# Optimization experiments

Measured on AMD Instinct MI355X. Metric: run time of the kernel, lower is better.

## Reference

```python
import jax, jax.numpy as jnp
import numpy as np

DIM = 64          # hidden dim
EDGE_DIM = 6      # edge feature dim
A = 6             # action_dim (torsion bins); also torsions per graph
B = 512           # num_graphs
NPG = 40          # nodes per graph
N = B * NPG       # 20480 nodes
E = 43008         # edges
T = B * A         # 3072 total torsions


def _lin_init(k, out_f, in_f):
    bound = 1.0 / np.sqrt(in_f)
    kw, kb = jax.random.split(k)
    w = jax.random.uniform(kw, (out_f, in_f), jnp.float32, -bound, bound)
    b = jax.random.uniform(kb, (out_f,), jnp.float32, -bound, bound)
    return w, b


def setup_inputs() -> dict:
    key = jax.random.key(0)
    ks = jax.random.split(key, 24)
    inp = {}
    inp['x'] = jax.random.normal(ks[0], (N, 3), jnp.float32)
    inp['edge_attr'] = jax.random.uniform(ks[1], (E, EDGE_DIM), jnp.float32)
    inp['edge_index'] = jax.random.randint(ks[2], (2, E), 0, N)
    inp['batch'] = jnp.arange(N, dtype=jnp.int32) // NPG            # graph-sorted
    inp['nrbidx'] = jnp.repeat(jnp.arange(B, dtype=jnp.int32), A)   # torsion -> graph
    inp['nonring'] = jax.random.randint(ks[3], (T, 4), 0, N)        # 4 atoms per torsion
    # parameters
    inp['lin0_w'], inp['lin0_b'] = _lin_init(ks[4], DIM, 3)
    inp['enn1_w'], inp['enn1_b'] = _lin_init(ks[5], DIM, EDGE_DIM)
    inp['enn2_w'], inp['enn2_b'] = _lin_init(ks[6], DIM * DIM, DIM)
    inp['root_w'] = jax.random.uniform(ks[7], (DIM, DIM), jnp.float32, -1/np.sqrt(DIM), 1/np.sqrt(DIM))
    inp['conv_b'] = jnp.zeros((DIM,), jnp.float32)
    inp['gru_w_ih'], inp['gru_b_ih'] = _lin_init(ks[8], 3 * DIM, DIM)
    inp['gru_w_hh'], inp['gru_b_hh'] = _lin_init(ks[9], 3 * DIM, DIM)
    inp['s2s_w_ih'], inp['s2s_b_ih'] = _lin_init(ks[10], 4 * DIM, 2 * DIM)
    inp['s2s_w_hh'], inp['s2s_b_hh'] = _lin_init(ks[11], 4 * DIM, DIM)
    inp['mem_w_ih'], inp['mem_b_ih'] = _lin_init(ks[12], 4 * DIM, 2 * DIM)
    inp['mem_w_hh'], inp['mem_b_hh'] = _lin_init(ks[13], 4 * DIM, DIM)
    inp['lin1_w'], inp['lin1_b'] = _lin_init(ks[14], DIM, 5 * DIM)
    inp['lin2_w'], inp['lin2_b'] = _lin_init(ks[15], A, DIM)
    return inp


def _lstm_cell(xin, hc, w_ih, w_hh, b_ih, b_hh):
    h, c = hc
    g = xin @ w_ih.T + b_ih + h @ w_hh.T + b_hh
    i, f, gg, o = jnp.split(g, 4, axis=-1)
    c2 = jax.nn.sigmoid(f) * c + jax.nn.sigmoid(i) * jnp.tanh(gg)
    h2 = jax.nn.sigmoid(o) * jnp.tanh(c2)
    return h2, (h2, c2)


def reference(x, edge_attr, lin0_w, lin0_b, enn1_w, enn1_b, enn2_w, enn2_b,
              root_w, conv_b, gru_w_ih, gru_b_ih, gru_w_hh, gru_b_hh,
              s2s_w_ih, s2s_b_ih, s2s_w_hh, s2s_b_hh,
              mem_w_ih, mem_b_ih, mem_w_hh, mem_b_hh,
              lin1_w, lin1_b, lin2_w, lin2_b,
              edge_index, batch, nrbidx, nonring):
    dim = DIM
    out = jax.nn.relu(x @ lin0_w.T + lin0_b)                         # (N, dim)
    # edge-conditioned weights (constant across the 6 iterations)
    ew = jax.nn.relu(edge_attr @ enn1_w.T + enn1_b)
    W = (ew @ enn2_w.T + enn2_b).reshape(-1, dim, dim)               # (E, dim, dim)
    src, dst = edge_index[0], edge_index[1]
    deg = jax.ops.segment_sum(jnp.ones_like(src, jnp.float32), dst, num_segments=N)
    denom = jnp.maximum(deg, 1.0)[:, None]
    h = out                                                          # GRU hidden
    for _ in range(6):
        msg = jnp.einsum('ei,eio->eo', out[src], W)                  # gather + bmm
        agg = jax.ops.segment_sum(msg, dst, num_segments=N) / denom  # scatter-mean
        m = jax.nn.relu(agg + out @ root_w + conv_b)                 # NNConv out
        gi = m @ gru_w_ih.T + gru_b_ih
        gh = h @ gru_w_hh.T + gru_b_hh
        ir, iz, inn = jnp.split(gi, 3, axis=-1)
        hr, hz, hn = jnp.split(gh, 3, axis=-1)
        r = jax.nn.sigmoid(ir + hr)
        z = jax.nn.sigmoid(iz + hz)
        n = jnp.tanh(inn + r * hn)
        h = (1.0 - z) * n + z * h
        out = h
    # Set2Set pooling (processing_steps=6)
    q_star = jnp.zeros((B, 2 * dim), out.dtype)
    hc = (jnp.zeros((B, dim), out.dtype), jnp.zeros((B, dim), out.dtype))
    for _ in range(6):
        q, hc = _lstm_cell(q_star, hc, s2s_w_ih, s2s_w_hh, s2s_b_ih, s2s_b_hh)
        e = jnp.sum(out * q[batch], axis=-1)                         # (N,)
        emax = jax.ops.segment_max(e, batch, num_segments=B)
        a = jnp.exp(e - emax[batch])
        a = a / jax.ops.segment_sum(a, batch, num_segments=B)[batch]
        r = jax.ops.segment_sum(a[:, None] * out, batch, num_segments=B)
        q_star = jnp.concatenate([q, r], axis=-1)                    # (B, 2*dim)
    # memory LSTM, one step, zero initial state
    hc0 = (jnp.zeros((B, dim), out.dtype), jnp.zeros((B, dim), out.dtype))
    lstm_out, (hx, cx) = _lstm_cell(q_star, hc0, mem_w_ih, mem_w_hh, mem_b_ih, mem_b_hh)
    t = lstm_out[nrbidx].reshape(B, 1, A, dim)
    nd = out[nonring.reshape(-1)].reshape(B, 4, A, dim)
    z2 = jnp.concatenate([t, nd], axis=1)                            # (B, 5, A, dim)
    z2 = jnp.transpose(z2, (0, 3, 2, 1)).reshape(-1, 5 * dim)        # (T, 5*dim)
    z2 = jax.nn.relu(z2 @ lin1_w.T + lin1_b)
    z2 = z2 @ lin2_w.T + lin2_b                                      # (T, A)
    logit = z2.reshape(B, A, A)   # equal torsion counts -> pad_sequence == reshape
    return (logit, hx[None], cx[None])
```

## Files before the change

kernel.cpp:

```cpp
#include <hip/hip_runtime.h>
#include <hip/hip_fp16.h>

#define NN 20480
#define EE 43008
#define BB 512
#define TT 3072

typedef _Float16 f16;
typedef _Float16 f16x8 __attribute__((ext_vector_type(8)));
typedef float f32x4 __attribute__((ext_vector_type(4)));

__device__ __forceinline__ float sigm(float x) { return 1.0f / (1.0f + __expf(-x)); }
__device__ __forceinline__ float tanh_f(float x) {
    float xc = fminf(fmaxf(x, -15.f), 15.f);
    float t = __expf(2.f * xc);
    return (t - 1.f) / (t + 1.f);
}

__global__ void k_prep0(const float* __restrict__ x, const float* __restrict__ ea,
                        const float* __restrict__ l0w, const float* __restrict__ l0b,
                        const float* __restrict__ e1w, const float* __restrict__ e1b,
                        const float* __restrict__ e2w, const float* __restrict__ e2b,
                        const float* __restrict__ gwih, const float* __restrict__ gwhh,
                        const float* __restrict__ swih, const float* __restrict__ swhh,
                        const float* __restrict__ mwih,
                        float* __restrict__ feat, f16* __restrict__ feat16, f16* __restrict__ ew16,
                        f16* __restrict__ qmtp, float* __restrict__ deg,
                        float* __restrict__ wihT, float* __restrict__ whhT,
                        float* __restrict__ s2sihT, float* __restrict__ s2shhT,
                        float* __restrict__ memihT)
{
    const int S0 = NN;
    const int S1 = S0 + NN * 64;
    const int S2 = S1 + EE * 64;
    const int S3 = S2 + 130 * 256 * 8;
    const int S4 = S3 + 64 * 192;
    const int S5 = S4 + 64 * 192;
    const int S6 = S5 + 128 * 256;
    const int S7 = S6 + 64 * 256;
    const int S8 = S7 + 128 * 256;
    for (int idx = blockIdx.x * blockDim.x + threadIdx.x; idx < S8; idx += gridDim.x * blockDim.x) {
        if (idx < S0) {
            deg[idx] = 0.f;
        } else if (idx < S1) {
            int t = idx - S0; int n = t >> 6, o = t & 63;
            float v = l0b[o] + x[n * 3] * l0w[o * 3] + x[n * 3 + 1] * l0w[o * 3 + 1] + x[n * 3 + 2] * l0w[o * 3 + 2];
            v = fmaxf(v, 0.f);
            feat[t] = v; feat16[t] = (f16)v;
        } else if (idx < S2) {
            int t = idx - S1; int e = t >> 6, o = t & 63;
            float acc = e1b[o];
#pragma unroll
            for (int j = 0; j < 6; ++j) acc += ea[e * 6 + j] * e1w[o * 6 + j];
            ew16[t] = (f16)fmaxf(acc, 0.f);
        } else if (idx < S3) {
            int t = idx - S2;
            int j = t & 7;
            int lane = (t >> 3) & 63;
            int cc = t >> 9;
            int c = cc >> 2, ct = cc & 3;
            int n = (ct << 4) | (lane & 15);
            int col = c * 32 + ((lane >> 4) << 3) + j;
            float v;
            if (col < 4096) v = e2w[(((col >> 6) << 6) + n) * 64 + (col & 63)];
            else            v = e2b[(col - 4096) * 64 + n];
            qmtp[t] = (f16)v;
        } else if (idx < S4) { int t = idx - S3; int i = t / 192, g = t - i * 192; wihT[t] = gwih[g * 64 + i]; }
        else if (idx < S5)   { int t = idx - S4; int i = t / 192, g = t - i * 192; whhT[t] = gwhh[g * 64 + i]; }
        else if (idx < S6)   { int t = idx - S5; int k = t >> 8, j = t & 255; s2sihT[t] = swih[j * 128 + k]; }
        else if (idx < S7)   { int t = idx - S6; int k = t >> 8, j = t & 255; s2shhT[t] = swhh[j * 64 + k]; }
        else                 { int t = idx - S7; int k = t >> 8, j = t & 255; memihT[t] = mwih[j * 128 + k]; }
    }
}

__global__ void k_prep1(const int* __restrict__ dstp, float* __restrict__ deg)
{
    int e = blockIdx.x * blockDim.x + threadIdx.x;
    if (e < EE) atomicAdd(&deg[dstp[e]], 1.0f);
}

__global__ __launch_bounds__(1024) void k_scan(const float* __restrict__ deg,
                                               int* __restrict__ rowptr, int* __restrict__ fill)
{
    __shared__ int part[1024];
    const int t = threadIdx.x;
    const int base = t * 20;
    int local[20];
    int s = 0;
#pragma unroll
    for (int j = 0; j < 20; ++j) { local[j] = s; s += (int)deg[base + j]; }
    part[t] = s;
    __syncthreads();
    for (int off = 1; off < 1024; off <<= 1) {
        int u = (t >= off) ? part[t - off] : 0;
        __syncthreads();
        part[t] += u;
        __syncthreads();
    }
    const int coff = part[t] - s;
#pragma unroll
    for (int j = 0; j < 20; ++j) { rowptr[base + j] = coff + local[j]; fill[base + j] = 0; }
    if (t == 1023) rowptr[NN] = part[1023];
}

__global__ void k_fill(const int* __restrict__ dstp, const int* __restrict__ rowptr,
                       int* __restrict__ fill, int* __restrict__ eidx)
{
    int e = blockIdx.x * blockDim.x + threadIdx.x;
    if (e < EE) {
        int d = dstp[e];
        int slot = atomicAdd(&fill[d], 1);
        eidx[rowptr[d] + slot] = e;
    }
}

__global__ __launch_bounds__(256, 3) void k_msg(const f16* __restrict__ feat16, const f16* __restrict__ ew16,
                                                const f16* __restrict__ qmtp,
                                                const int* __restrict__ srcp,
                                                float* __restrict__ msg)
{
    __shared__ f16 s_lds[64 * 64];
    __shared__ f16 w_lds[64 * 64];
    __shared__ float cmb[2][64][36];
    const int tid = threadIdx.x;
    const int e0 = blockIdx.x * 64;
    {
        int row = tid >> 2, q = tid & 3;
        int sn = srcp[e0 + row];
        const uint4* gs = (const uint4*)(feat16 + (size_t)sn * 64 + q * 16);
        const uint4* gw = (const uint4*)(ew16 + (size_t)(e0 + row) * 64 + q * 16);
        uint4 s0v = gs[0], s1v = gs[1];
        uint4 w0v = gw[0], w1v = gw[1];
        char* sbw = (char*)s_lds;
        char* wbw = (char*)w_lds;
        int swz = (row & 7) << 4;
        *(uint4*)(sbw + row * 128 + ((q * 32) ^ swz)) = s0v;
        *(uint4*)(sbw + row * 128 + ((q * 32 + 16) ^ swz)) = s1v;
        *(uint4*)(wbw + row * 128 + ((q * 32) ^ swz)) = w0v;
        *(uint4*)(wbw + row * 128 + ((q * 32 + 16) ^ swz)) = w1v;
    }
    __syncthreads();
    const int wv = tid >> 6, l = tid & 63;
    const int lh = l >> 4, ll = l & 15;
    const int cp = wv & 1;
    const int kp = wv >> 1;
    const int ctb = cp * 2;
    const char* sb = (const char*)s_lds;
    const char* wb = (const char*)w_lds;
    int rowv[4], swzv[4];
#pragma unroll
    for (int rg = 0; rg < 4; ++rg) { rowv[rg] = rg * 16 + ll; swzv[rg] = (rowv[rg] & 7) << 4; }
    f16x8 wf[4][2];
#pragma unroll
    for (int rg = 0; rg < 4; ++rg) {
        wf[rg][0] = *(const f16x8*)(wb + rowv[rg] * 128 + ((lh * 16) ^ swzv[rg]));
        wf[rg][1] = *(const f16x8*)(wb + rowv[rg] * 128 + ((64 + lh * 16) ^ swzv[rg]));
    }
    const f16x8* base = (const f16x8*)qmtp + l;
    f32x4 acc[4][2] = {};
    const int i0 = kp * 32;
    f16x8 S[3][2][2];
#pragma unroll
    for (int pp = 0; pp < 3; ++pp)
#pragma unroll
        for (int ab = 0; ab < 2; ++ab)
#pragma unroll
            for (int j = 0; j < 2; ++j)
                S[pp][ab][j] = base[((2 * (i0 + pp) + ab) * 4 + ctb + j) * 64];
    f16x8 sc[4];
#pragma unroll
    for (int p = 0; p < 32; ++p) {
        if ((p & 7) == 0) {
#pragma unroll
            for (int rg = 0; rg < 4; ++rg)
                sc[rg] = *(const f16x8*)(sb + rowv[rg] * 128 + ((((i0 + p) * 2)) ^ swzv[rg]));
        }
        const int bi = p % 3;
        __builtin_amdgcn_s_setprio(1);
#pragma unroll
        for (int rg = 0; rg < 4; ++rg) {
            f16 s = sc[rg][p & 7];
            f16x8 a0, a1;
#pragma unroll
            for (int j8 = 0; j8 < 8; ++j8) { a0[j8] = wf[rg][0][j8] * s; a1[j8] = wf[rg][1][j8] * s; }
#pragma unroll
            for (int j = 0; j < 2; ++j) {
                acc[rg][j] = __builtin_amdgcn_mfma_f32_16x16x32_f16(a0, S[bi][0][j], acc[rg][j], 0, 0, 0);
                acc[rg][j] = __builtin_amdgcn_mfma_f32_16x16x32_f16(a1, S[bi][1][j], acc[rg][j], 0, 0, 0);
            }
        }
        __builtin_amdgcn_s_setprio(0);
        int inext = i0 + p + 3; if (inext > 64) inext = 64;
#pragma unroll
        for (int ab = 0; ab < 2; ++ab)
#pragma unroll
            for (int j = 0; j < 2; ++j)
                S[bi][ab][j] = base[((2 * inext + ab) * 4 + ctb + j) * 64];
    }
    if (kp == 1) {
#pragma unroll
        for (int rg = 0; rg < 4; ++rg) {
            f16x8 sf0 = *(const f16x8*)(sb + rowv[rg] * 128 + ((lh * 16) ^ swzv[rg]));
            f16x8 sf1 = *(const f16x8*)(sb + rowv[rg] * 128 + ((64 + lh * 16) ^ swzv[rg]));
#pragma unroll
            for (int j = 0; j < 2; ++j) {
                acc[rg][j] = __builtin_amdgcn_mfma_f32_16x16x32_f16(sf0, S[2][0][j], acc[rg][j], 0, 0, 0);
                acc[rg][j] = __builtin_amdgcn_mfma_f32_16x16x32_f16(sf1, S[2][1][j], acc[rg][j], 0, 0, 0);
            }
        }
#pragma unroll
        for (int rg = 0; rg < 4; ++rg)
#pragma unroll
            for (int j = 0; j < 2; ++j)
#pragma unroll
                for (int q = 0; q < 4; ++q)
                    cmb[cp][rg * 16 + lh * 4 + q][j * 16 + ll] = acc[rg][j][q];
    }
    __syncthreads();
    if (kp == 0) {
#pragma unroll
        for (int rg = 0; rg < 4; ++rg)
#pragma unroll
            for (int q = 0; q < 4; ++q) {
                int r = rg * 16 + lh * 4 + q;
#pragma unroll
                for (int j = 0; j < 2; ++j) {
                    float v = acc[rg][j][q] + cmb[cp][r][j * 16 + ll];
                    msg[(size_t)(e0 + r) * 64 + ctb * 16 + j * 16 + ll] = v;
                }
            }
    }
}

__global__ __launch_bounds__(256) void k_node(float* __restrict__ feat, f16* __restrict__ feat16,
                                              const float* __restrict__ msg, const int* __restrict__ rowptr,
                                              const int* __restrict__ eidx, const float* __restrict__ deg,
                                              const float* __restrict__ root_w, const float* __restrict__ conv_b,
                                              const float* __restrict__ wihT, const float* __restrict__ whhT,
                                              const float* __restrict__ bih, const float* __restrict__ bhh)
{
    __shared__ float h_lds[4][4][64];
    __shared__ float m_lds[4][4][64];
    const int wv = threadIdx.x >> 6, l = threadIdx.x & 63;
    const int nb = blockIdx.x * 16 + wv * 4;
    float h[4], m[4];
#pragma unroll
    for (int nd = 0; nd < 4; ++nd) {
        int n = nb + nd;
        float hv = feat[(size_t)n * 64 + l];
        h[nd] = hv; h_lds[wv][nd][l] = hv;
        int r0 = rowptr[n], r1 = rowptr[n + 1];
        float a = 0.f;
        for (int r = r0; r < r1; ++r) {
            int e = eidx[r];
            a += msg[(size_t)e * 64 + l];
        }
        float inv = 1.0f / fmaxf(deg[n], 1.0f);
        m[nd] = a * inv + conv_b[l];
    }
    __syncthreads();
    for (int i = 0; i < 64; ++i) {
        float w = root_w[i * 64 + l];
#pragma unroll
        for (int nd = 0; nd < 4; ++nd) m[nd] += h_lds[wv][nd][i] * w;
    }
#pragma unroll
    for (int nd = 0; nd < 4; ++nd) { m[nd] = fmaxf(m[nd], 0.f); m_lds[wv][nd][l] = m[nd]; }
    __syncthreads();
    float g0[4], g1[4], g2[4], G0[4], G1[4], G2[4];
#pragma unroll
    for (int nd = 0; nd < 4; ++nd) {
        g0[nd] = bih[l]; g1[nd] = bih[64 + l]; g2[nd] = bih[128 + l];
        G0[nd] = bhh[l]; G1[nd] = bhh[64 + l]; G2[nd] = bhh[128 + l];
    }
    for (int i = 0; i < 64; ++i) {
        float wi0 = wihT[i * 192 + l], wi1 = wihT[i * 192 + 64 + l], wi2 = wihT[i * 192 + 128 + l];
        float wh0 = whhT[i * 192 + l], wh1 = whhT[i * 192 + 64 + l], wh2 = whhT[i * 192 + 128 + l];
#pragma unroll
        for (int nd = 0; nd < 4; ++nd) {
            float mb = m_lds[wv][nd][i], hb = h_lds[wv][nd][i];
            g0[nd] += mb * wi0; g1[nd] += mb * wi1; g2[nd] += mb * wi2;
            G0[nd] += hb * wh0; G1[nd] += hb * wh1; G2[nd] += hb * wh2;
        }
    }
#pragma unroll
    for (int nd = 0; nd < 4; ++nd) {
        int n = nb + nd;
        float r = sigm(g0[nd] + G0[nd]);
        float z = sigm(g1[nd] + G1[nd]);
        float nn2 = tanh_f(g2[nd] + r * G2[nd]);
        float hn = (1.f - z) * nn2 + z * h[nd];
        feat[(size_t)n * 64 + l] = hn;
        feat16[(size_t)n * 64 + l] = (f16)hn;
    }
}

__global__ __launch_bounds__(512) void k_s2s(const float* __restrict__ feat,
                                             const float* __restrict__ s2sihT, const float* __restrict__ s2shhT,
                                             const float* __restrict__ sbih, const float* __restrict__ sbhh,
                                             const float* __restrict__ memihT,
                                             const float* __restrict__ mbih, const float* __restrict__ mbhh,
                                             float* __restrict__ lstm_out, float* __restrict__ dout)
{
    __shared__ float ft[2][64][49];
    __shared__ float qs[2][128];
    __shared__ float hh[2][64];
    __shared__ float cc[2][64];
    __shared__ float qv[2][64];
    __shared__ float g0p[2][256];
    __shared__ float g1p[2][256];
    const int t = threadIdx.x;
    const int g0 = blockIdx.x * 2;
    for (int i = t; i < 2 * 40 * 64; i += 512) {
        int g = i / 2560;
        int rem = i - g * 2560;
        int row = rem >> 6, o = rem & 63;
        ft[g][o][row] = feat[((size_t)(g0 + g) * 40 + row) * 64 + o];
    }
    if (t < 256) qs[t >> 7][t & 127] = 0.f;
    if (t < 128) { hh[t >> 6][t & 63] = 0.f; cc[t >> 6][t & 63] = 0.f; }
    __syncthreads();
    const int jj = t & 255;
    const int half = t >> 8;
    const int gg = t >> 6, gl = t & 63;
    const float b_s = sbih[jj] + sbhh[jj];
    const float b_m = mbih[jj] + mbhh[jj];
    for (int step = 0; step < 7; ++step) {
        const bool mem = (step == 6);
        {
            float a0, a1;
            if (!mem) {
                if (half == 0) {
                    a0 = b_s; a1 = b_s;
#pragma unroll 16
                    for (int k = 0; k < 96; ++k) {
                        float w = s2sihT[k * 256 + jj];
                        a0 += qs[0][k] * w;
                        a1 += qs[1][k] * w;
                    }
                } else {
                    a0 = 0.f; a1 = 0.f;
#pragma unroll 16
                    for (int k = 96; k < 128; ++k) {
                        float w = s2sihT[k * 256 + jj];
                        a0 += qs[0][k] * w;
                        a1 += qs[1][k] * w;
                    }
#pragma unroll 16
                    for (int k = 0; k < 64; ++k) {
                        float w = s2shhT[k * 256 + jj];
                        a0 += hh[0][k] * w;
                        a1 += hh[1][k] * w;
                    }
                }
            } else {
                if (half == 0) {
                    a0 = b_m; a1 = b_m;
#pragma unroll 16
                    for (int k = 0; k < 64; ++k) {
                        float w = memihT[k * 256 + jj];
                        a0 += qs[0][k] * w;
                        a1 += qs[1][k] * w;
                    }
                } else {
                    a0 = 0.f; a1 = 0.f;
#pragma unroll 16
                    for (int k = 64; k < 128; ++k) {
                        float w = memihT[k * 256 + jj];
                        a0 += qs[0][k] * w;
                        a1 += qs[1][k] * w;
                    }
                }
            }
            if (half == 0) { g0p[0][jj] = a0; g0p[1][jj] = a1; }
            else           { g1p[0][jj] = a0; g1p[1][jj] = a1; }
        }
        __syncthreads();
        if (t < 128) {
            float ii = sigm(g0p[gg][gl]        + g1p[gg][gl]);
            float ff = sigm(g0p[gg][64 + gl]   + g1p[gg][64 + gl]);
            float g2 = tanh_f(g0p[gg][128 + gl] + g1p[gg][128 + gl]);
            float oo = sigm(g0p[gg][192 + gl]  + g1p[gg][192 + gl]);
            float cprev = mem ? 0.f : cc[gg][gl];
            float c2 = ff * cprev + ii * g2;
            float h2 = oo * tanh_f(c2);
            if (!mem) {
                cc[gg][gl] = c2; hh[gg][gl] = h2;
                qv[gg][gl] = h2; qs[gg][gl] = h2;
                const int g = gg, l = gl;
                float e = -1e30f;
                if (l < 40) {
                    float s = 0.f;
                    for (int o = 0; o < 64; ++o) s += ft[g][o][l] * qv[g][o];
                    e = s;
                }
                float emax = e;
#pragma unroll
                for (int off = 32; off; off >>= 1) emax = fmaxf(emax, __shfl_xor(emax, off));
                float av = (l < 40) ? __expf(e - emax) : 0.f;
                float asum = av;
#pragma unroll
                for (int off = 32; off; off >>= 1) asum += __shfl_xor(asum, off);
                av /= asum;
                float r = 0.f;
                for (int nd = 0; nd < 40; ++nd) r += __shfl(av, nd) * ft[g][l][nd];
                qs[g][64 + l] = r;
            } else {
                int gidx = g0 + gg;
                lstm_out[(size_t)gidx * 64 + gl] = h2;
                dout[18432 + (size_t)gidx * 64 + gl] = h2;
                dout[18432 + 32768 + (size_t)gidx * 64 + gl] = c2;
            }
        }
        __syncthreads();
    }
}

__global__ __launch_bounds__(256) void k_final(const float* __restrict__ feat,
                                               const float* __restrict__ lstm_out,
                                               const int* __restrict__ nrbidx, const int* __restrict__ nonring,
                                               const float* __restrict__ l1w, const float* __restrict__ l1b,
                                               const float* __restrict__ l2w, const float* __restrict__ l2b,
                                               float* __restrict__ dout)
{
    __shared__ float z_lds[4][320];
    __shared__ float y_lds[4][64];
    const int wv = threadIdx.x >> 6, l = threadIdx.x & 63;
    const int r = blockIdx.x * 4 + wv;
    const int b = r / 6, rr = r - b * 6;
#pragma unroll
    for (int p = 0; p < 5; ++p) {
        int c = p * 64 + l;
        int f2 = rr * 320 + c;
        int d = f2 / 30;
        int rem = f2 - d * 30;
        int a = rem / 5;
        int s = rem - a * 5;
        float v;
        if (s == 0) v = lstm_out[(size_t)nrbidx[b * 6 + a] * 64 + d];
        else {
            int atom = nonring[b * 24 + (s - 1) * 6 + a];
            v = feat[(size_t)atom * 64 + d];
        }
        z_lds[wv][c] = v;
    }
    __syncthreads();
    {
        float acc = l1b[l];
        const float4* wr = (const float4*)(l1w + (size_t)l * 320);
        const float4* zr = (const float4*)(z_lds[wv]);
        for (int c4 = 0; c4 < 80; ++c4) {
            float4 w4 = wr[c4]; float4 z4 = zr[c4];
            acc += w4.x * z4.x + w4.y * z4.y + w4.z * z4.z + w4.w * z4.w;
        }
        y_lds[wv][l] = fmaxf(acc, 0.f);
    }
    __syncthreads();
    if (l < 6) {
        float acc = l2b[l];
        const float* yr = y_lds[wv];
        const float* w2 = l2w + l * 64;
        for (int o = 0; o < 64; ++o) acc += yr[o] * w2[o];
        dout[b * 36 + rr * 6 + l] = acc;
    }
}

extern "C" void kernel_launch(void* const* d_in, const int* in_sizes, int n_in,
                              void* d_out, int out_size, void* d_ws, size_t ws_size,
                              hipStream_t stream)
{
    const float* x    = (const float*)d_in[0];
    const float* ea   = (const float*)d_in[1];
    const int*   ei   = (const int*)d_in[2];
    const int*   nrb  = (const int*)d_in[4];
    const int*   nonr = (const int*)d_in[5];
    const float* l0w  = (const float*)d_in[6];  const float* l0b = (const float*)d_in[7];
    const float* e1w  = (const float*)d_in[8];  const float* e1b = (const float*)d_in[9];
    const float* e2w  = (const float*)d_in[10]; const float* e2b = (const float*)d_in[11];
    const float* rootw= (const float*)d_in[12]; const float* convb = (const float*)d_in[13];
    const float* gwih = (const float*)d_in[14]; const float* gbih = (const float*)d_in[15];
    const float* gwhh = (const float*)d_in[16]; const float* gbhh = (const float*)d_in[17];
    const float* swih = (const float*)d_in[18]; const float* sbih = (const float*)d_in[19];
    const float* swhh = (const float*)d_in[20]; const float* sbhh = (const float*)d_in[21];
    const float* mwih = (const float*)d_in[22]; const float* mbih = (const float*)d_in[23];
    const float* mbhh = (const float*)d_in[25];
    const float* l1w  = (const float*)d_in[26]; const float* l1b = (const float*)d_in[27];
    const float* l2w  = (const float*)d_in[28]; const float* l2b = (const float*)d_in[29];
    const int* srcp = ei;
    const int* dstp = ei + EE;
    float* dout = (float*)d_out;

    char* w = (char*)d_ws;
    size_t off = 0;
    auto alloc = [&](size_t bytes) -> void* {
        off = (off + 255) & ~(size_t)255;
        void* p = w + off;
        off += bytes;
        return p;
    };
    float* feat    = (float*)alloc((size_t)NN * 64 * 4);
    f16*   feat16  = (f16*)alloc((size_t)NN * 64 * 2);
    f16*   ew16    = (f16*)alloc((size_t)EE * 64 * 2);
    f16*   qmtp    = (f16*)alloc((size_t)132 * 256 * 8 * 2);
    float* msg     = (float*)alloc((size_t)EE * 64 * 4);
    float* deg     = (float*)alloc((size_t)NN * 4);
    int*   rowptr  = (int*)alloc((size_t)(NN + 1) * 4);
    int*   fill    = (int*)alloc((size_t)NN * 4);
    int*   eidx    = (int*)alloc((size_t)EE * 4);
    float* wihT    = (float*)alloc((size_t)64 * 192 * 4);
    float* whhT    = (float*)alloc((size_t)64 * 192 * 4);
    float* s2sihT  = (float*)alloc((size_t)128 * 256 * 4);
    float* s2shhT  = (float*)alloc((size_t)64 * 256 * 4);
    float* memihT  = (float*)alloc((size_t)128 * 256 * 4);
    float* lstmo   = (float*)alloc((size_t)BB * 64 * 4);
    (void)ws_size; (void)in_sizes; (void)n_in; (void)out_size;

    hipLaunchKernelGGL(k_prep0, dim3(1024), dim3(256), 0, stream,
                       x, ea, l0w, l0b, e1w, e1b, e2w, e2b, gwih, gwhh, swih, swhh, mwih,
                       feat, feat16, ew16, qmtp, deg, wihT, whhT, s2sihT, s2shhT, memihT);
    hipLaunchKernelGGL(k_prep1, dim3(EE / 256), dim3(256), 0, stream, dstp, deg);
    hipLaunchKernelGGL(k_scan, dim3(1), dim3(1024), 0, stream, deg, rowptr, fill);
    hipLaunchKernelGGL(k_fill, dim3(EE / 256), dim3(256), 0, stream, dstp, rowptr, fill, eidx);
    for (int it = 0; it < 6; ++it) {
        hipLaunchKernelGGL(k_msg, dim3(EE / 64), dim3(256), 0, stream,
                           feat16, ew16, qmtp, srcp, msg);
        hipLaunchKernelGGL(k_node, dim3(NN / 16), dim3(256), 0, stream,
                           feat, feat16, msg, rowptr, eidx, deg, rootw, convb, wihT, whhT, gbih, gbhh);
    }
    hipLaunchKernelGGL(k_s2s, dim3(BB / 2), dim3(512), 0, stream,
                       feat, s2sihT, s2shhT, sbih, sbhh, memihT, mbih, mbhh, lstmo, dout);
    hipLaunchKernelGGL(k_final, dim3(TT / 4), dim3(256), 0, stream,
                       feat, lstmo, nrb, nonr, l1w, l1b, l2w, l2b, dout);
}
```

Measured before the change: 424.9 us.

## Stage edge-network weight tiles through double-buffered LDS in message kernel

The message kernel now runs 512 threads per block, with each wave owning a 16-edge row group and a 32-column half, instead of splitting the K dimension across waves and combining partials in LDS. The shared qmtp weight tensor is streamed cooperatively into a double-buffered LDS tile, one 16 KB stage per step, rather than each wave loading it from global memory into registers. This removes redundant per-wave global weight traffic and the final partial-sum reduction. The cost is a __syncthreads on every one of the 32 stages and LDS read pressure from the B operands.

```diff
diff --git a/kernel.cpp b/kernel.cpp
--- a/kernel.cpp
+++ b/kernel.cpp
@@ -114,121 +114,105 @@
     }
 }
 
-__global__ __launch_bounds__(256, 3) void k_msg(const f16* __restrict__ feat16, const f16* __restrict__ ew16,
+__global__ __launch_bounds__(512, 4) void k_msg(const f16* __restrict__ feat16, const f16* __restrict__ ew16,
                                                 const f16* __restrict__ qmtp,
                                                 const int* __restrict__ srcp,
                                                 float* __restrict__ msg)
 {
     __shared__ f16 s_lds[64 * 64];
     __shared__ f16 w_lds[64 * 64];
-    __shared__ float cmb[2][64][36];
+    __shared__ char bls[2][16384];
     const int tid = threadIdx.x;
     const int e0 = blockIdx.x * 64;
+    const char* qb = (const char*)qmtp;
     {
-        int row = tid >> 2, q = tid & 3;
+        int row = tid >> 3, seg = tid & 7;
         int sn = srcp[e0 + row];
-        const uint4* gs = (const uint4*)(feat16 + (size_t)sn * 64 + q * 16);
-        const uint4* gw = (const uint4*)(ew16 + (size_t)(e0 + row) * 64 + q * 16);
-        uint4 s0v = gs[0], s1v = gs[1];
-        uint4 w0v = gw[0], w1v = gw[1];
-        char* sbw = (char*)s_lds;
-        char* wbw = (char*)w_lds;
-        int swz = (row & 7) << 4;
-        *(uint4*)(sbw + row * 128 + ((q * 32) ^ swz)) = s0v;
-        *(uint4*)(sbw + row * 128 + ((q * 32 + 16) ^ swz)) = s1v;
-        *(uint4*)(wbw + row * 128 + ((q * 32) ^ swz)) = w0v;
-        *(uint4*)(wbw + row * 128 + ((q * 32 + 16) ^ swz)) = w1v;
-    }
-    __syncthreads();
+        uint4 sv = *(const uint4*)(feat16 + (size_t)sn * 64 + seg * 8);
+        uint4 wv4 = *(const uint4*)(ew16 + (size_t)(e0 + row) * 64 + seg * 8);
+        int swz0 = (row & 7) << 4;
+        *(uint4*)((char*)s_lds + row * 128 + ((seg * 16) ^ swz0)) = sv;
+        *(uint4*)((char*)w_lds + row * 128 + ((seg * 16) ^ swz0)) = wv4;
+    }
+    {
+        uint4 r0 = *(const uint4*)(qb + tid * 32);
+        uint4 r1 = *(const uint4*)(qb + tid * 32 + 16);
+        *(uint4*)(bls[0] + tid * 32) = r0;
+        *(uint4*)(bls[0] + tid * 32 + 16) = r1;
+    }
+    __syncthreads();
+
     const int wv = tid >> 6, l = tid & 63;
     const int lh = l >> 4, ll = l & 15;
-    const int cp = wv & 1;
-    const int kp = wv >> 1;
-    const int ctb = cp * 2;
+    const int eg = wv >> 1, cp = wv & 1;
+    const int row = eg * 16 + ll;
+    const int swz = (row & 7) << 4;
     const char* sb = (const char*)s_lds;
     const char* wb = (const char*)w_lds;
-    int rowv[4], swzv[4];
-#pragma unroll
-    for (int rg = 0; rg < 4; ++rg) { rowv[rg] = rg * 16 + ll; swzv[rg] = (rowv[rg] & 7) << 4; }
-    f16x8 wf[4][2];
-#pragma unroll
-    for (int rg = 0; rg < 4; ++rg) {
-        wf[rg][0] = *(const f16x8*)(wb + rowv[rg] * 128 + ((lh * 16) ^ swzv[rg]));
-        wf[rg][1] = *(const f16x8*)(wb + rowv[rg] * 128 + ((64 + lh * 16) ^ swzv[rg]));
-    }
-    const f16x8* base = (const f16x8*)qmtp + l;
-    f32x4 acc[4][2] = {};
-    const int i0 = kp * 32;
-    f16x8 S[3][2][2];
-#pragma unroll
-    for (int pp = 0; pp < 3; ++pp)
-#pragma unroll
-        for (int ab = 0; ab < 2; ++ab)
-#pragma unroll
-            for (int j = 0; j < 2; ++j)
-                S[pp][ab][j] = base[((2 * (i0 + pp) + ab) * 4 + ctb + j) * 64];
-    f16x8 sc[4];
-#pragma unroll
-    for (int p = 0; p < 32; ++p) {
-        if ((p & 7) == 0) {
-#pragma unroll
-            for (int rg = 0; rg < 4; ++rg)
-                sc[rg] = *(const f16x8*)(sb + rowv[rg] * 128 + ((((i0 + p) * 2)) ^ swzv[rg]));
-        }
-        const int bi = p % 3;
-        __builtin_amdgcn_s_setprio(1);
-#pragma unroll
-        for (int rg = 0; rg < 4; ++rg) {
-            f16 s = sc[rg][p & 7];
-            f16x8 a0, a1;
-#pragma unroll
-            for (int j8 = 0; j8 < 8; ++j8) { a0[j8] = wf[rg][0][j8] * s; a1[j8] = wf[rg][1][j8] * s; }
-#pragma unroll
-            for (int j = 0; j < 2; ++j) {
-                acc[rg][j] = __builtin_amdgcn_mfma_f32_16x16x32_f16(a0, S[bi][0][j], acc[rg][j], 0, 0, 0);
-                acc[rg][j] = __builtin_amdgcn_mfma_f32_16x16x32_f16(a1, S[bi][1][j], acc[rg][j], 0, 0, 0);
-            }
-        }
-        __builtin_amdgcn_s_setprio(0);
-        int inext = i0 + p + 3; if (inext > 64) inext = 64;
-#pragma unroll
-        for (int ab = 0; ab < 2; ++ab)
-#pragma unroll
-            for (int j = 0; j < 2; ++j)
-                S[bi][ab][j] = base[((2 * inext + ab) * 4 + ctb + j) * 64];
-    }
-    if (kp == 1) {
-#pragma unroll
-        for (int rg = 0; rg < 4; ++rg) {
-            f16x8 sf0 = *(const f16x8*)(sb + rowv[rg] * 128 + ((lh * 16) ^ swzv[rg]));
-            f16x8 sf1 = *(const f16x8*)(sb + rowv[rg] * 128 + ((64 + lh * 16) ^ swzv[rg]));
-#pragma unroll
-            for (int j = 0; j < 2; ++j) {
-                acc[rg][j] = __builtin_amdgcn_mfma_f32_16x16x32_f16(sf0, S[2][0][j], acc[rg][j], 0, 0, 0);
-                acc[rg][j] = __builtin_amdgcn_mfma_f32_16x16x32_f16(sf1, S[2][1][j], acc[rg][j], 0, 0, 0);
-            }
-        }
-#pragma unroll
-        for (int rg = 0; rg < 4; ++rg)
-#pragma unroll
-            for (int j = 0; j < 2; ++j)
-#pragma unroll
-                for (int q = 0; q < 4; ++q)
-                    cmb[cp][rg * 16 + lh * 4 + q][j * 16 + ll] = acc[rg][j][q];
-    }
-    __syncthreads();
-    if (kp == 0) {
-#pragma unroll
-        for (int rg = 0; rg < 4; ++rg)
-#pragma unroll
-            for (int q = 0; q < 4; ++q) {
-                int r = rg * 16 + lh * 4 + q;
-#pragma unroll
-                for (int j = 0; j < 2; ++j) {
-                    float v = acc[rg][j][q] + cmb[cp][r][j * 16 + ll];
-                    msg[(size_t)(e0 + r) * 64 + ctb * 16 + j * 16 + ll] = v;
+    f16x8 wf[2];
+    wf[0] = *(const f16x8*)(wb + row * 128 + ((lh * 16) ^ swz));
+    wf[1] = *(const f16x8*)(wb + row * 128 + ((64 + lh * 16) ^ swz));
+    f32x4 acc[2] = {};
+
+    for (int to = 0; to < 8; ++to) {
+        f16x8 sc = *(const f16x8*)(sb + row * 128 + ((to * 16) ^ swz));
+#pragma unroll
+        for (int u = 0; u < 4; ++u) {
+            const int t = to * 4 + u;
+            uint4 n0, n1;
+            bool havestage;
+            if (t < 31) {
+                havestage = true;
+                n0 = *(const uint4*)(qb + (size_t)(t + 1) * 16384 + tid * 32);
+                n1 = *(const uint4*)(qb + (size_t)(t + 1) * 16384 + tid * 32 + 16);
+            } else {
+                havestage = (tid < 256);
+                if (havestage) {
+                    n0 = *(const uint4*)(qb + (size_t)32 * 16384 + tid * 32);
+                    n1 = *(const uint4*)(qb + (size_t)32 * 16384 + tid * 32 + 16);
                 }
             }
+            const char* bp = bls[u & 1];
+            __builtin_amdgcn_s_setprio(1);
+#pragma unroll
+            for (int cl = 0; cl < 4; ++cl) {
+                f16 s = sc[2 * u + (cl >> 1)];
+                f16x8 wsel = wf[cl & 1];
+                f16x8 a;
+#pragma unroll
+                for (int j8 = 0; j8 < 8; ++j8) a[j8] = wsel[j8] * s;
+                f16x8 b0 = *(const f16x8*)(bp + (cl * 4 + cp * 2) * 1024 + l * 16);
+                f16x8 b1 = *(const f16x8*)(bp + (cl * 4 + cp * 2 + 1) * 1024 + l * 16);
+                acc[0] = __builtin_amdgcn_mfma_f32_16x16x32_f16(a, b0, acc[0], 0, 0, 0);
+                acc[1] = __builtin_amdgcn_mfma_f32_16x16x32_f16(a, b1, acc[1], 0, 0, 0);
+            }
+            __builtin_amdgcn_s_setprio(0);
+            if (havestage) {
+                *(uint4*)(bls[(u & 1) ^ 1] + tid * 32) = n0;
+                *(uint4*)(bls[(u & 1) ^ 1] + tid * 32 + 16) = n1;
+            }
+            __syncthreads();
+        }
+    }
+    {
+        f16x8 sf0 = *(const f16x8*)(sb + row * 128 + ((lh * 16) ^ swz));
+        f16x8 sf1 = *(const f16x8*)(sb + row * 128 + ((64 + lh * 16) ^ swz));
+        const char* bp = bls[0];
+        f16x8 b00 = *(const f16x8*)(bp + (0 * 4 + cp * 2) * 1024 + l * 16);
+        f16x8 b01 = *(const f16x8*)(bp + (0 * 4 + cp * 2 + 1) * 1024 + l * 16);
+        f16x8 b10 = *(const f16x8*)(bp + (1 * 4 + cp * 2) * 1024 + l * 16);
+        f16x8 b11 = *(const f16x8*)(bp + (1 * 4 + cp * 2 + 1) * 1024 + l * 16);
+        acc[0] = __builtin_amdgcn_mfma_f32_16x16x32_f16(sf0, b00, acc[0], 0, 0, 0);
+        acc[1] = __builtin_amdgcn_mfma_f32_16x16x32_f16(sf0, b01, acc[1], 0, 0, 0);
+        acc[0] = __builtin_amdgcn_mfma_f32_16x16x32_f16(sf1, b10, acc[0], 0, 0, 0);
+        acc[1] = __builtin_amdgcn_mfma_f32_16x16x32_f16(sf1, b11, acc[1], 0, 0, 0);
+    }
+#pragma unroll
+    for (int q = 0; q < 4; ++q) {
+        int r = eg * 16 + lh * 4 + q;
+        float* mp = msg + (size_t)(e0 + r) * 64 + cp * 32;
+        mp[ll] = acc[0][q];
+        mp[16 + ll] = acc[1][q];
     }
 }
 
@@ -522,7 +506,7 @@
     hipLaunchKernelGGL(k_scan, dim3(1), dim3(1024), 0, stream, deg, rowptr, fill);
     hipLaunchKernelGGL(k_fill, dim3(EE / 256), dim3(256), 0, stream, dstp, rowptr, fill, eidx);
     for (int it = 0; it < 6; ++it) {
-        hipLaunchKernelGGL(k_msg, dim3(EE / 64), dim3(256), 0, stream,
+        hipLaunchKernelGGL(k_msg, dim3(EE / 64), dim3(512), 0, stream,
                            feat16, ew16, qmtp, srcp, msg);
         hipLaunchKernelGGL(k_node, dim3(NN / 16), dim3(256), 0, stream,
                            feat, feat16, msg, rowptr, eidx, deg, rootw, convb, wihT, whhT, gbih, gbhh);
```

Result: slower. 478.5 us (+12.6%).

## Use fp16 MFMA for root and GRU matmuls in node update kernel

Applied to the files above, without the earlier changes.

Rewrites the per-node update so the root-weight projection and both GRU gate matmuls run on 16x16x32 fp16 MFMA. Each wave now handles 16 nodes, with swizzled LDS tiles for the hidden and message operands and weights pre-packed into MFMA fragment layout in the prep kernel. This replaces scalar fp32 FMA loops that reloaded weights from global memory, at the cost of fp16 rounding of the hidden state and weights and fewer blocks per launch.

```diff
diff --git a/kernel.cpp b/kernel.cpp
--- a/kernel.cpp
+++ b/kernel.cpp
@@ -21,12 +21,13 @@
                         const float* __restrict__ l0w, const float* __restrict__ l0b,
                         const float* __restrict__ e1w, const float* __restrict__ e1b,
                         const float* __restrict__ e2w, const float* __restrict__ e2b,
+                        const float* __restrict__ rootw,
                         const float* __restrict__ gwih, const float* __restrict__ gwhh,
                         const float* __restrict__ swih, const float* __restrict__ swhh,
                         const float* __restrict__ mwih,
                         float* __restrict__ feat, f16* __restrict__ feat16, f16* __restrict__ ew16,
                         f16* __restrict__ qmtp, float* __restrict__ deg,
-                        float* __restrict__ wihT, float* __restrict__ whhT,
+                        f16* __restrict__ rootp, f16* __restrict__ wihp, f16* __restrict__ whhp,
                         float* __restrict__ s2sihT, float* __restrict__ s2shhT,
                         float* __restrict__ memihT)
 {
@@ -34,12 +35,13 @@
     const int S1 = S0 + NN * 64;
     const int S2 = S1 + EE * 64;
     const int S3 = S2 + 130 * 256 * 8;
-    const int S4 = S3 + 64 * 192;
-    const int S5 = S4 + 64 * 192;
-    const int S6 = S5 + 128 * 256;
-    const int S7 = S6 + 64 * 256;
-    const int S8 = S7 + 128 * 256;
-    for (int idx = blockIdx.x * blockDim.x + threadIdx.x; idx < S8; idx += gridDim.x * blockDim.x) {
+    const int S4 = S3 + 4096;
+    const int S5 = S4 + 12288;
+    const int S6 = S5 + 12288;
+    const int S7 = S6 + 128 * 256;
+    const int S8 = S7 + 64 * 256;
+    const int S9 = S8 + 128 * 256;
+    for (int idx = blockIdx.x * blockDim.x + threadIdx.x; idx < S9; idx += gridDim.x * blockDim.x) {
         if (idx < S0) {
             deg[idx] = 0.f;
         } else if (idx < S1) {
@@ -65,11 +67,31 @@
             if (col < 4096) v = e2w[(((col >> 6) << 6) + n) * 64 + (col & 63)];
             else            v = e2b[(col - 4096) * 64 + n];
             qmtp[t] = (f16)v;
-        } else if (idx < S4) { int t = idx - S3; int i = t / 192, g = t - i * 192; wihT[t] = gwih[g * 64 + i]; }
-        else if (idx < S5)   { int t = idx - S4; int i = t / 192, g = t - i * 192; whhT[t] = gwhh[g * 64 + i]; }
-        else if (idx < S6)   { int t = idx - S5; int k = t >> 8, j = t & 255; s2sihT[t] = swih[j * 128 + k]; }
-        else if (idx < S7)   { int t = idx - S6; int k = t >> 8, j = t & 255; s2shhT[t] = swhh[j * 64 + k]; }
-        else                 { int t = idx - S7; int k = t >> 8, j = t & 255; memihT[t] = mwih[j * 128 + k]; }
+        } else if (idx < S4) {
+            int t = idx - S3; int j = t & 7; int lane = (t >> 3) & 63;
+            int cc = t >> 9;
+            int ct = cc >> 1, c = cc & 1;
+            int n = ct * 16 + (lane & 15);
+            int k = c * 32 + ((lane >> 4) << 3) + j;
+            rootp[t] = (f16)rootw[k * 64 + n];
+        } else if (idx < S5) {
+            int t = idx - S4; int j = t & 7; int lane = (t >> 3) & 63;
+            int cc = t >> 9;
+            int gct = cc >> 1, c = cc & 1;
+            int g = gct * 16 + (lane & 15);
+            int k = c * 32 + ((lane >> 4) << 3) + j;
+            wihp[t] = (f16)gwih[g * 64 + k];
+        } else if (idx < S6) {
+            int t = idx - S5; int j = t & 7; int lane = (t >> 3) & 63;
+            int cc = t >> 9;
+            int gct = cc >> 1, c = cc & 1;
+            int g = gct * 16 + (lane & 15);
+            int k = c * 32 + ((lane >> 4) << 3) + j;
+            whhp[t] = (f16)gwhh[g * 64 + k];
+        }
+        else if (idx < S7)   { int t = idx - S6; int k = t >> 8, j = t & 255; s2sihT[t] = swih[j * 128 + k]; }
+        else if (idx < S8)   { int t = idx - S7; int k = t >> 8, j = t & 255; s2shhT[t] = swhh[j * 64 + k]; }
+        else                 { int t = idx - S8; int k = t >> 8, j = t & 255; memihT[t] = mwih[j * 128 + k]; }
     }
 }
 
@@ -233,65 +255,98 @@
 }
 
 __global__ __launch_bounds__(256) void k_node(float* __restrict__ feat, f16* __restrict__ feat16,
-                                              const float* __restrict__ msg, const int* __restrict__ rowptr,
-                                              const int* __restrict__ eidx, const float* __restrict__ deg,
-                                              const float* __restrict__ root_w, const float* __restrict__ conv_b,
-                                              const float* __restrict__ wihT, const float* __restrict__ whhT,
-                                              const float* __restrict__ bih, const float* __restrict__ bhh)
-{
-    __shared__ float h_lds[4][4][64];
-    __shared__ float m_lds[4][4][64];
+        const float* __restrict__ msg, const int* __restrict__ rowptr,
+        const int* __restrict__ eidx, const float* __restrict__ deg,
+        const f16* __restrict__ rootp, const f16* __restrict__ wihp, const f16* __restrict__ whhp,
+        const float* __restrict__ conv_b, const float* __restrict__ bih, const float* __restrict__ bhh)
+{
+    __shared__ f16 h16s[4][16 * 64];
+    __shared__ f16 m16s[4][16 * 64];
+    __shared__ float aggm[4][16][68];
     const int wv = threadIdx.x >> 6, l = threadIdx.x & 63;
-    const int nb = blockIdx.x * 16 + wv * 4;
-    float h[4], m[4];
-#pragma unroll
-    for (int nd = 0; nd < 4; ++nd) {
-        int n = nb + nd;
+    const int lh = l >> 4, ll = l & 15;
+    const int nbw = blockIdx.x * 64 + wv * 16;
+    char* hb = (char*)h16s[wv];
+    char* mb = (char*)m16s[wv];
+    for (int nd = 0; nd < 16; ++nd) {
+        int n = nbw + nd;
         float hv = feat[(size_t)n * 64 + l];
-        h[nd] = hv; h_lds[wv][nd][l] = hv;
         int r0 = rowptr[n], r1 = rowptr[n + 1];
         float a = 0.f;
-        for (int r = r0; r < r1; ++r) {
-            int e = eidx[r];
-            a += msg[(size_t)e * 64 + l];
-        }
-        float inv = 1.0f / fmaxf(deg[n], 1.0f);
-        m[nd] = a * inv + conv_b[l];
-    }
-    __syncthreads();
-    for (int i = 0; i < 64; ++i) {
-        float w = root_w[i * 64 + l];
-#pragma unroll
-        for (int nd = 0; nd < 4; ++nd) m[nd] += h_lds[wv][nd][i] * w;
-    }
-#pragma unroll
-    for (int nd = 0; nd < 4; ++nd) { m[nd] = fmaxf(m[nd], 0.f); m_lds[wv][nd][l] = m[nd]; }
-    __syncthreads();
-    float g0[4], g1[4], g2[4], G0[4], G1[4], G2[4];
-#pragma unroll
-    for (int nd = 0; nd < 4; ++nd) {
-        g0[nd] = bih[l]; g1[nd] = bih[64 + l]; g2[nd] = bih[128 + l];
-        G0[nd] = bhh[l]; G1[nd] = bhh[64 + l]; G2[nd] = bhh[128 + l];
-    }
-    for (int i = 0; i < 64; ++i) {
-        float wi0 = wihT[i * 192 + l], wi1 = wihT[i * 192 + 64 + l], wi2 = wihT[i * 192 + 128 + l];
-        float wh0 = whhT[i * 192 + l], wh1 = whhT[i * 192 + 64 + l], wh2 = whhT[i * 192 + 128 + l];
-#pragma unroll
-        for (int nd = 0; nd < 4; ++nd) {
-            float mb = m_lds[wv][nd][i], hb = h_lds[wv][nd][i];
-            g0[nd] += mb * wi0; g1[nd] += mb * wi1; g2[nd] += mb * wi2;
-            G0[nd] += hb * wh0; G1[nd] += hb * wh1; G2[nd] += hb * wh2;
-        }
-    }
-#pragma unroll
-    for (int nd = 0; nd < 4; ++nd) {
-        int n = nb + nd;
-        float r = sigm(g0[nd] + G0[nd]);
-        float z = sigm(g1[nd] + G1[nd]);
-        float nn2 = tanh_f(g2[nd] + r * G2[nd]);
-        float hn = (1.f - z) * nn2 + z * h[nd];
-        feat[(size_t)n * 64 + l] = hn;
-        feat16[(size_t)n * 64 + l] = (f16)hn;
+        for (int r = r0; r < r1; ++r) a += msg[(size_t)eidx[r] * 64 + l];
+        aggm[wv][nd][l] = a;
+        int swz = (nd & 7) << 4;
+        *(f16*)(hb + nd * 128 + ((l * 2) ^ swz)) = (f16)hv;
+    }
+    __syncthreads();
+    const int rsw = (ll & 7) << 4;
+    f16x8 hA0 = *(const f16x8*)(hb + ll * 128 + ((lh * 16) ^ rsw));
+    f16x8 hA1 = *(const f16x8*)(hb + ll * 128 + ((64 + lh * 16) ^ rsw));
+    float invd[4];
+#pragma unroll
+    for (int q = 0; q < 4; ++q) invd[q] = 1.0f / fmaxf(deg[nbw + lh * 4 + q], 1.0f);
+#pragma unroll
+    for (int ct = 0; ct < 4; ++ct) {
+        f16x8 b0 = *(const f16x8*)(rootp + ((size_t)(ct * 2 + 0) * 64 + l) * 8);
+        f16x8 b1 = *(const f16x8*)(rootp + ((size_t)(ct * 2 + 1) * 64 + l) * 8);
+        f32x4 acc = {};
+        acc = __builtin_amdgcn_mfma_f32_16x16x32_f16(hA0, b0, acc, 0, 0, 0);
+        acc = __builtin_amdgcn_mfma_f32_16x16x32_f16(hA1, b1, acc, 0, 0, 0);
+        int col = ct * 16 + ll;
+        float cb = conv_b[col];
+#pragma unroll
+        for (int q = 0; q < 4; ++q) {
+            int row = lh * 4 + q;
+            float mv = fmaxf(aggm[wv][row][col] * invd[q] + acc[q] + cb, 0.f);
+            int swz = (row & 7) << 4;
+            *(f16*)(mb + row * 128 + ((col * 2) ^ swz)) = (f16)mv;
+        }
+    }
+    __syncthreads();
+    f16x8 mA0 = *(const f16x8*)(mb + ll * 128 + ((lh * 16) ^ rsw));
+    f16x8 mA1 = *(const f16x8*)(mb + ll * 128 + ((64 + lh * 16) ^ rsw));
+#pragma unroll
+    for (int ct = 0; ct < 4; ++ct) {
+        f32x4 gi0 = {}, gi1 = {}, gi2 = {}, gh0 = {}, gh1 = {}, gh2 = {};
+        f16x8 b;
+        b = *(const f16x8*)(wihp + ((size_t)((ct + 0) * 2 + 0) * 64 + l) * 8);
+        gi0 = __builtin_amdgcn_mfma_f32_16x16x32_f16(mA0, b, gi0, 0, 0, 0);
+        b = *(const f16x8*)(wihp + ((size_t)((ct + 0) * 2 + 1) * 64 + l) * 8);
+        gi0 = __builtin_amdgcn_mfma_f32_16x16x32_f16(mA1, b, gi0, 0, 0, 0);
+        b = *(const f16x8*)(wihp + ((size_t)((ct + 4) * 2 + 0) * 64 + l) * 8);
+        gi1 = __builtin_amdgcn_mfma_f32_16x16x32_f16(mA0, b, gi1, 0, 0, 0);
+        b = *(const f16x8*)(wihp + ((size_t)((ct + 4) * 2 + 1) * 64 + l) * 8);
+        gi1 = __builtin_amdgcn_mfma_f32_16x16x32_f16(mA1, b, gi1, 0, 0, 0);
+        b = *(const f16x8*)(wihp + ((size_t)((ct + 8) * 2 + 0) * 64 + l) * 8);
+        gi2 = __builtin_amdgcn_mfma_f32_16x16x32_f16(mA0, b, gi2, 0, 0, 0);
+        b = *(const f16x8*)(wihp + ((size_t)((ct + 8) * 2 + 1) * 64 + l) * 8);
+        gi2 = __builtin_amdgcn_mfma_f32_16x16x32_f16(mA1, b, gi2, 0, 0, 0);
+        b = *(const f16x8*)(whhp + ((size_t)((ct + 0) * 2 + 0) * 64 + l) * 8);
+        gh0 = __builtin_amdgcn_mfma_f32_16x16x32_f16(hA0, b, gh0, 0, 0, 0);
+        b = *(const f16x8*)(whhp + ((size_t)((ct + 0) * 2 + 1) * 64 + l) * 8);
+        gh0 = __builtin_amdgcn_mfma_f32_16x16x32_f16(hA1, b, gh0, 0, 0, 0);
+        b = *(const f16x8*)(whhp + ((size_t)((ct + 4) * 2 + 0) * 64 + l) * 8);
+        gh1 = __builtin_amdgcn_mfma_f32_16x16x32_f16(hA0, b, gh1, 0, 0, 0);
+        b = *(const f16x8*)(whhp + ((size_t)((ct + 4) * 2 + 1) * 64 + l) * 8);
+        gh1 = __builtin_amdgcn_mfma_f32_16x16x32_f16(hA1, b, gh1, 0, 0, 0);
+        b = *(const f16x8*)(whhp + ((size_t)((ct + 8) * 2 + 0) * 64 + l) * 8);
+        gh2 = __builtin_amdgcn_mfma_f32_16x16x32_f16(hA0, b, gh2, 0, 0, 0);
+        b = *(const f16x8*)(whhp + ((size_t)((ct + 8) * 2 + 1) * 64 + l) * 8);
+        gh2 = __builtin_amdgcn_mfma_f32_16x16x32_f16(hA1, b, gh2, 0, 0, 0);
+        int col = ct * 16 + ll;
+        float bi0 = bih[col], bi1 = bih[64 + col], bi2 = bih[128 + col];
+        float bh0 = bhh[col], bh1 = bhh[64 + col], bh2 = bhh[128 + col];
+#pragma unroll
+        for (int q = 0; q < 4; ++q) {
+            int n = nbw + lh * 4 + q;
+            float r = sigm(gi0[q] + bi0 + gh0[q] + bh0);
+            float z = sigm(gi1[q] + bi1 + gh1[q] + bh1);
+            float nn2 = tanh_f(gi2[q] + bi2 + r * (gh2[q] + bh2));
+            float hold = feat[(size_t)n * 64 + col];
+            float hn = (1.f - z) * nn2 + z * hold;
+            feat[(size_t)n * 64 + col] = hn;
+            feat16[(size_t)n * 64 + col] = (f16)hn;
+        }
     }
 }
 
@@ -507,8 +562,9 @@
     int*   rowptr  = (int*)alloc((size_t)(NN + 1) * 4);
     int*   fill    = (int*)alloc((size_t)NN * 4);
     int*   eidx    = (int*)alloc((size_t)EE * 4);
-    float* wihT    = (float*)alloc((size_t)64 * 192 * 4);
-    float* whhT    = (float*)alloc((size_t)64 * 192 * 4);
+    f16*   rootp   = (f16*)alloc((size_t)4096 * 2);
+    f16*   wihp    = (f16*)alloc((size_t)12288 * 2);
+    f16*   whhp    = (f16*)alloc((size_t)12288 * 2);
     float* s2sihT  = (float*)alloc((size_t)128 * 256 * 4);
     float* s2shhT  = (float*)alloc((size_t)64 * 256 * 4);
     float* memihT  = (float*)alloc((size_t)128 * 256 * 4);
@@ -516,16 +572,16 @@
     (void)ws_size; (void)in_sizes; (void)n_in; (void)out_size;
 
     hipLaunchKernelGGL(k_prep0, dim3(1024), dim3(256), 0, stream,
-                       x, ea, l0w, l0b, e1w, e1b, e2w, e2b, gwih, gwhh, swih, swhh, mwih,
-                       feat, feat16, ew16, qmtp, deg, wihT, whhT, s2sihT, s2shhT, memihT);
+                       x, ea, l0w, l0b, e1w, e1b, e2w, e2b, rootw, gwih, gwhh, swih, swhh, mwih,
+                       feat, feat16, ew16, qmtp, deg, rootp, wihp, whhp, s2sihT, s2shhT, memihT);
     hipLaunchKernelGGL(k_prep1, dim3(EE / 256), dim3(256), 0, stream, dstp, deg);
     hipLaunchKernelGGL(k_scan, dim3(1), dim3(1024), 0, stream, deg, rowptr, fill);
     hipLaunchKernelGGL(k_fill, dim3(EE / 256), dim3(256), 0, stream, dstp, rowptr, fill, eidx);
     for (int it = 0; it < 6; ++it) {
         hipLaunchKernelGGL(k_msg, dim3(EE / 64), dim3(256), 0, stream,
                            feat16, ew16, qmtp, srcp, msg);
-        hipLaunchKernelGGL(k_node, dim3(NN / 16), dim3(256), 0, stream,
-                           feat, feat16, msg, rowptr, eidx, deg, rootw, convb, wihT, whhT, gbih, gbhh);
+        hipLaunchKernelGGL(k_node, dim3(NN / 64), dim3(256), 0, stream,
+                           feat, feat16, msg, rowptr, eidx, deg, rootp, wihp, whhp, convb, gbih, gbhh);
     }
     hipLaunchKernelGGL(k_s2s, dim3(BB / 2), dim3(512), 0, stream,
                        feat, s2sihT, s2shhT, sbih, sbhh, memihT, mbih, mbhh, lstmo, dout);
```

Measured after the change: 467.0 us. 9.9% more time.
